# Kernel tuning notes

Hardware: AMD Instinct MI355X
Metric: run time of the kernel (lower is better)

## Reference

```python
import jax, jax.numpy as jnp
import numpy as np

N_BINS = 15
N = 20_000_000


def setup_inputs() -> dict:
    key = jax.random.key(0)
    k1, k2, k3 = jax.random.split(key, 3)
    preds = jax.random.randint(k1, (N,), 0, 1000, dtype=jnp.int64)
    targets = jax.random.randint(k2, (N,), 0, 1000, dtype=jnp.int64)
    confs = jax.random.uniform(k3, (N,), dtype=jnp.float32)
    return {"preds": preds, "targets": targets, "confs": confs}


def reference(preds, targets, confs):
    n = confs.shape[0]
    acc = (preds == targets).astype(confs.dtype)
    # bin i covers (i/n_bins, (i+1)/n_bins]; conf <= 0 falls in no bin
    idx = jnp.ceil(confs * N_BINS).astype(jnp.int32) - 1
    valid = idx >= 0
    idx = jnp.where(valid, idx, 0)
    w = valid.astype(confs.dtype)
    count = jax.ops.segment_sum(w, idx, num_segments=N_BINS)
    conf_sum = jax.ops.segment_sum(confs * w, idx, num_segments=N_BINS)
    acc_sum = jax.ops.segment_sum(acc * w, idx, num_segments=N_BINS)
    prop = count / n
    safe = jnp.maximum(count, 1.0)
    gap = jnp.abs(conf_sum / safe - acc_sum / safe)
    ece = jnp.sum(jnp.where(count > 0, gap * prop, 0.0))
    return ece.reshape(1)
```

## Files before the change

### kernel.cpp

```cpp
#include <hip/hip_runtime.h>

#define ECE_BINS 15
#define NTHREADS 256
#define NBLOCKS  768

__global__ __launch_bounds__(256) void ece_fused_kernel(
    const int* __restrict__ preds,
    const int* __restrict__ targets,
    const float* __restrict__ confs,
    int n,
    unsigned long long* __restrict__ ws,
    float* __restrict__ out)
{
    unsigned cnt[ECE_BINS];
    double   cf[ECE_BINS];
    #pragma unroll
    for (int b = 0; b < ECE_BINS; ++b) { cnt[b] = 0u; cf[b] = 0.0; }

    const long tid = (long)blockIdx.x * NTHREADS + threadIdx.x;
    const long S   = (long)gridDim.x * NTHREADS;
    const int nvec = n >> 2;
    const int4*   p4 = (const int4*)preds;
    const int4*   t4 = (const int4*)targets;
    const float4* c4 = (const float4*)confs;

    for (long i = tid; i < nvec; i += S) {
        int4 p = p4[i]; int4 t = t4[i]; float4 c = c4[i];
        const int   pv[4] = {p.x, p.y, p.z, p.w};
        const int   tv[4] = {t.x, t.y, t.z, t.w};
        const float cv[4] = {c.x, c.y, c.z, c.w};
        #pragma unroll
        for (int j = 0; j < 4; ++j) {
            int idx = (int)ceilf(cv[j] * 15.0f) - 1;
            unsigned inc = (pv[j] == tv[j]) ? 0x10001u : 1u;
            double qd = trunc((double)cv[j] * 4294967296.0);
            #pragma unroll
            for (int b = 0; b < ECE_BINS; ++b) {
                bool m = (idx == b);
                cnt[b] += m ? inc : 0u;
                cf[b]  += m ? qd : 0.0;
            }
        }
    }
    for (long k = ((long)nvec << 2) + tid; k < n; k += S) {
        int idx = (int)ceilf(confs[k] * 15.0f) - 1;
        unsigned inc = (preds[k] == targets[k]) ? 0x10001u : 1u;
        double qd = trunc((double)confs[k] * 4294967296.0);
        #pragma unroll
        for (int b = 0; b < ECE_BINS; ++b) {
            bool m = (idx == b);
            cnt[b] += m ? inc : 0u;
            cf[b]  += m ? qd : 0.0;
        }
    }

    __shared__ unsigned s_cnt[NTHREADS][ECE_BINS];
    __shared__ double   s_cf [NTHREADS][ECE_BINS];
    #pragma unroll
    for (int b = 0; b < ECE_BINS; ++b) {
        s_cnt[threadIdx.x][b] = cnt[b];
        s_cf [threadIdx.x][b] = cf[b];
    }
    __syncthreads();

    unsigned c1 = 0; double d1 = 0.0; int b1 = 0, k1 = 0;
    if (threadIdx.x < 240) {
        b1 = threadIdx.x % 15; k1 = threadIdx.x / 15;
        #pragma unroll
        for (int m = 0; m < 16; ++m) {
            c1 += s_cnt[k1 * 16 + m][b1];
            d1 += s_cf [k1 * 16 + m][b1];
        }
    }
    __syncthreads();
    if (threadIdx.x < 240) { s_cnt[k1][b1] = c1; s_cf[k1][b1] = d1; }
    __syncthreads();

    if (threadIdx.x < ECE_BINS) {
        const int b = threadIdx.x;
        unsigned cs = 0; double ds = 0.0;
        #pragma unroll
        for (int m = 0; m < 16; ++m) { cs += s_cnt[m][b]; ds += s_cf[m][b]; }
        unsigned long long count = cs & 0xFFFFu;
        unsigned long long corr  = cs >> 16;
        atomicAdd(&ws[b],      count | (corr << 32));
        atomicAdd(&ws[15 + b], (unsigned long long)ds);
        __threadfence();
    }
    __syncthreads();

    if (threadIdx.x == 0) {
        unsigned long long t = atomicAdd(&ws[30], 1ull);
        if (t == (unsigned long long)gridDim.x - 1ull) {
            double ece = 0.0;
            for (int b = 0; b < ECE_BINS; ++b) {
                unsigned long long ca = atomicAdd(&ws[b], 0ull);
                unsigned long long cq = atomicAdd(&ws[15 + b], 0ull);
                double c = (double)(unsigned)(ca & 0xffffffffull);
                double a = (double)(unsigned)(ca >> 32);
                double s = (double)cq * (1.0 / 4294967296.0);
                if (c > 0.0) ece += fabs(s / c - a / c) * (c / (double)n);
            }
            out[0] = (float)ece;
        }
    }
}

extern "C" void kernel_launch(void* const* d_in, const int* in_sizes, int n_in,
                              void* d_out, int out_size, void* d_ws, size_t ws_size,
                              hipStream_t stream) {
    const int*   preds   = (const int*)d_in[0];
    const int*   targets = (const int*)d_in[1];
    const float* confs   = (const float*)d_in[2];
    float*       out     = (float*)d_out;
    const int    n       = in_sizes[2];

    unsigned long long* ws = (unsigned long long*)d_ws;

    hipMemsetAsync(ws, 0, 31 * sizeof(unsigned long long), stream);

    ece_fused_kernel<<<NBLOCKS, NTHREADS, 0, stream>>>(preds, targets, confs, n, ws, out);
}
```

Baseline: 269.0 us.

## Replace per-thread register bin arrays with packed 64-bit shared-memory atomic histogram

Drops the 15-way per-thread compare-and-accumulate (including double-precision adds) and instead packs a quantized confidence, a count and a correctness flag into one 64-bit word. Each element does a single shared-memory atomicAdd into one of 64 sub-histograms. The grid grows from 768 to 2048 blocks, and the final reduction reads the workspace with atomic loads. This removes heavy FP64 ALU work, but shared 64-bit atomics can contend, and the packed fields can overflow: the count field is 10 bits per sub-slot, and the 42-bit confidence sum in a sub-slot with many entries may carry into the count bits.

```diff
diff --git a/kernel.cpp b/kernel.cpp
--- a/kernel.cpp
+++ b/kernel.cpp
@@ -2,7 +2,11 @@
 
 #define ECE_BINS 15
 #define NTHREADS 256
-#define NBLOCKS  768
+#define NBLOCKS  2048
+#define NSUB     64
+#define CNT_SHIFT 42
+#define COR_SHIFT 52
+#define CONF_MASK ((1ull << CNT_SHIFT) - 1)
 
 __global__ __launch_bounds__(256) void ece_fused_kernel(
     const int* __restrict__ preds,
@@ -12,11 +16,12 @@
     unsigned long long* __restrict__ ws,
     float* __restrict__ out)
 {
-    unsigned cnt[ECE_BINS];
-    double   cf[ECE_BINS];
-    #pragma unroll
-    for (int b = 0; b < ECE_BINS; ++b) { cnt[b] = 0u; cf[b] = 0.0; }
+    __shared__ unsigned long long hist[ECE_BINS + 1][NSUB];
+    for (int i = threadIdx.x; i < (ECE_BINS + 1) * NSUB; i += NTHREADS)
+        (&hist[0][0])[i] = 0ull;
+    __syncthreads();
 
+    const int  sub = threadIdx.x & (NSUB - 1);
     const long tid = (long)blockIdx.x * NTHREADS + threadIdx.x;
     const long S   = (long)gridDim.x * NTHREADS;
     const int nvec = n >> 2;
@@ -31,60 +36,38 @@
         const float cv[4] = {c.x, c.y, c.z, c.w};
         #pragma unroll
         for (int j = 0; j < 4; ++j) {
-            int idx = (int)ceilf(cv[j] * 15.0f) - 1;
-            unsigned inc = (pv[j] == tv[j]) ? 0x10001u : 1u;
-            double qd = trunc((double)cv[j] * 4294967296.0);
-            #pragma unroll
-            for (int b = 0; b < ECE_BINS; ++b) {
-                bool m = (idx == b);
-                cnt[b] += m ? inc : 0u;
-                cf[b]  += m ? qd : 0.0;
-            }
+            int i0  = (int)ceilf(cv[j] * 15.0f);
+            int row = (i0 <= 0) ? ECE_BINS : (i0 - 1);
+            unsigned q = (unsigned)(cv[j] * 4294967296.0f);
+            unsigned long long val = (unsigned long long)q | (1ull << CNT_SHIFT)
+                                   | ((pv[j] == tv[j]) ? (1ull << COR_SHIFT) : 0ull);
+            atomicAdd(&hist[row][sub], val);
         }
     }
     for (long k = ((long)nvec << 2) + tid; k < n; k += S) {
-        int idx = (int)ceilf(confs[k] * 15.0f) - 1;
-        unsigned inc = (preds[k] == targets[k]) ? 0x10001u : 1u;
-        double qd = trunc((double)confs[k] * 4294967296.0);
-        #pragma unroll
-        for (int b = 0; b < ECE_BINS; ++b) {
-            bool m = (idx == b);
-            cnt[b] += m ? inc : 0u;
-            cf[b]  += m ? qd : 0.0;
-        }
+        float cf = confs[k];
+        int i0  = (int)ceilf(cf * 15.0f);
+        int row = (i0 <= 0) ? ECE_BINS : (i0 - 1);
+        unsigned q = (unsigned)(cf * 4294967296.0f);
+        unsigned long long val = (unsigned long long)q | (1ull << CNT_SHIFT)
+                               | ((preds[k] == targets[k]) ? (1ull << COR_SHIFT) : 0ull);
+        atomicAdd(&hist[row][sub], val);
     }
 
-    __shared__ unsigned s_cnt[NTHREADS][ECE_BINS];
-    __shared__ double   s_cf [NTHREADS][ECE_BINS];
-    #pragma unroll
-    for (int b = 0; b < ECE_BINS; ++b) {
-        s_cnt[threadIdx.x][b] = cnt[b];
-        s_cf [threadIdx.x][b] = cf[b];
-    }
     __syncthreads();
-
-    unsigned c1 = 0; double d1 = 0.0; int b1 = 0, k1 = 0;
-    if (threadIdx.x < 240) {
-        b1 = threadIdx.x % 15; k1 = threadIdx.x / 15;
-        #pragma unroll
-        for (int m = 0; m < 16; ++m) {
-            c1 += s_cnt[k1 * 16 + m][b1];
-            d1 += s_cf [k1 * 16 + m][b1];
-        }
-    }
-    __syncthreads();
-    if (threadIdx.x < 240) { s_cnt[k1][b1] = c1; s_cf[k1][b1] = d1; }
-    __syncthreads();
-
     if (threadIdx.x < ECE_BINS) {
         const int b = threadIdx.x;
-        unsigned cs = 0; double ds = 0.0;
-        #pragma unroll
-        for (int m = 0; m < 16; ++m) { cs += s_cnt[m][b]; ds += s_cf[m][b]; }
-        unsigned long long count = cs & 0xFFFFu;
-        unsigned long long corr  = cs >> 16;
-        atomicAdd(&ws[b],      count | (corr << 32));
-        atomicAdd(&ws[15 + b], (unsigned long long)ds);
+        unsigned long long csum = 0ull;
+        unsigned cnt = 0u, corr = 0u;
+        #pragma unroll 8
+        for (int s = 0; s < NSUB; ++s) {
+            unsigned long long v = hist[b][s];
+            csum += v & CONF_MASK;
+            cnt  += (unsigned)((v >> CNT_SHIFT) & 0x3FFull);
+            corr += (unsigned)(v >> COR_SHIFT);
+        }
+        atomicAdd(&ws[b],            (unsigned long long)cnt | ((unsigned long long)corr << 32));
+        atomicAdd(&ws[ECE_BINS + b], csum);
         __threadfence();
     }
     __syncthreads();
@@ -92,13 +75,20 @@
     if (threadIdx.x == 0) {
         unsigned long long t = atomicAdd(&ws[30], 1ull);
         if (t == (unsigned long long)gridDim.x - 1ull) {
+            __threadfence();
+            unsigned long long ca[ECE_BINS], cq[ECE_BINS];
+            #pragma unroll
+            for (int b = 0; b < ECE_BINS; ++b)
+                ca[b] = __hip_atomic_load(&ws[b], __ATOMIC_RELAXED, __HIP_MEMORY_SCOPE_AGENT);
+            #pragma unroll
+            for (int b = 0; b < ECE_BINS; ++b)
+                cq[b] = __hip_atomic_load(&ws[ECE_BINS + b], __ATOMIC_RELAXED, __HIP_MEMORY_SCOPE_AGENT);
             double ece = 0.0;
+            #pragma unroll
             for (int b = 0; b < ECE_BINS; ++b) {
-                unsigned long long ca = atomicAdd(&ws[b], 0ull);
-                unsigned long long cq = atomicAdd(&ws[15 + b], 0ull);
-                double c = (double)(unsigned)(ca & 0xffffffffull);
-                double a = (double)(unsigned)(ca >> 32);
-                double s = (double)cq * (1.0 / 4294967296.0);
+                double c = (double)(unsigned)(ca[b] & 0xffffffffull);
+                double a = (double)(unsigned)(ca[b] >> 32);
+                double s = (double)cq[b] * (1.0 / 4294967296.0);
                 if (c > 0.0) ece += fabs(s / c - a / c) * (c / (double)n);
             }
             out[0] = (float)ece;
@@ -116,7 +106,6 @@
     const int    n       = in_sizes[2];
 
     unsigned long long* ws = (unsigned long long*)d_ws;
-
     hipMemsetAsync(ws, 0, 31 * sizeof(unsigned long long), stream);
 
     ece_fused_kernel<<<NBLOCKS, NTHREADS, 0, stream>>>(preds, targets, confs, n, ws, out);
```

New measurement: 327.7 us. 21.8% more time.
